# Kernel tuning notes

Measured on AMD Instinct MI355X. Metric: run time of the kernel, lower is better.

## Reference

```python
import jax, jax.numpy as jnp
import numpy as np

MAX_RES = 10.0  # max_residue_magnitude
DG = 16         # deformable_groups
KH = KW = 3
PAD = 1


def conv3x3(x, w, b):
    y = jax.lax.conv_general_dilated(x, w, window_strides=(1, 1), padding='SAME',
                                     dimension_numbers=('NCHW', 'OIHW', 'NCHW'))
    return y + b[None, :, None, None]


def lrelu(x):
    return jnp.where(x >= 0, x, 0.1 * x)


def deform_conv2d(x, offset, mask, weight, bias):
    # x: [B,C,H,W]; offset: [B,2*DG*K,H,W] as (dy,dx) pairs; mask: [B,DG*K,H,W]
    B, C, H, W = x.shape
    Cout, Cin, kh, kw = weight.shape
    K = kh * kw
    Cg = C // DG
    ky, kx = jnp.meshgrid(jnp.arange(kh), jnp.arange(kw), indexing='ij')
    ky = (ky.reshape(K) - PAD).astype(x.dtype)
    kx = (kx.reshape(K) - PAD).astype(x.dtype)
    off = offset.reshape(B, DG, K, 2, H, W)
    m = mask.reshape(B, DG, K, H, W)
    hh = jnp.arange(H, dtype=x.dtype)[None, None, None, :, None]
    ww = jnp.arange(W, dtype=x.dtype)[None, None, None, None, :]
    ys = hh + ky[None, None, :, None, None] + off[:, :, :, 0]  # [B,DG,K,H,W]
    xs = ww + kx[None, None, :, None, None] + off[:, :, :, 1]
    xg = x.reshape(B, DG, Cg, H, W)

    def sample_one(img, ys1, xs1):
        # img [Cg,H,W], ys1/xs1 [K,H,W]; bilinear with zero outside
        y0 = jnp.floor(ys1)
        x0 = jnp.floor(xs1)
        wy = ys1 - y0
        wx = xs1 - x0
        y0i = y0.astype(jnp.int32)
        x0i = x0.astype(jnp.int32)

        def g(yi, xi):
            valid = ((yi >= 0) & (yi < H) & (xi >= 0) & (xi < W)).astype(img.dtype)
            yc = jnp.clip(yi, 0, H - 1)
            xc = jnp.clip(xi, 0, W - 1)
            return img[:, yc, xc] * valid[None]  # [Cg,K,H,W]

        v00 = g(y0i, x0i)
        v01 = g(y0i, x0i + 1)
        v10 = g(y0i + 1, x0i)
        v11 = g(y0i + 1, x0i + 1)
        return (v00 * (1 - wy) * (1 - wx) + v01 * (1 - wy) * wx
                + v10 * wy * (1 - wx) + v11 * wy * wx)

    sampled = jax.vmap(jax.vmap(sample_one))(xg, ys, xs)     # [B,DG,Cg,K,H,W]
    sampled = sampled * m[:, :, None]
    sampled = sampled.reshape(B, C, K, H, W)
    wk = weight.reshape(Cout, Cin, K)
    out = jnp.einsum('bckhw,ock->bohw', sampled, wk)
    return out + bias[None, :, None, None]


def setup_inputs() -> dict:
    key = jax.random.key(0)
    ks = jax.random.split(key, 12)
    B, C, H, W = 4, 64, 128, 128
    s = lambda fan: 1.0 / np.sqrt(fan)
    inp = {
        'x': jax.random.normal(ks[0], (B, C, H, W), jnp.float32),
        'x_flow_warped': jax.random.normal(ks[1], (B, C, H, W), jnp.float32),
        'x_current': jax.random.normal(ks[2], (B, C, H, W), jnp.float32),
        'flow': jax.random.normal(ks[3], (B, 2, H, W), jnp.float32) * 2.0,
        'w_off1': jax.random.normal(ks[4], (64, 130, 3, 3), jnp.float32) * s(130 * 9),
        'b_off1': jnp.zeros((64,), jnp.float32),
        'w_off2': jax.random.normal(ks[5], (64, 64, 3, 3), jnp.float32) * s(64 * 9),
        'b_off2': jnp.zeros((64,), jnp.float32),
        'w_off3': jax.random.normal(ks[6], (64, 64, 3, 3), jnp.float32) * s(64 * 9),
        'b_off3': jnp.zeros((64,), jnp.float32),
        'w_off4': jax.random.normal(ks[7], (432, 64, 3, 3), jnp.float32) * s(64 * 9),
        'b_off4': jnp.zeros((432,), jnp.float32),
        'dcn_w': jax.random.normal(ks[8], (64, 64, 3, 3), jnp.float32) * s(64 * 9),
        'dcn_b': jnp.zeros((64,), jnp.float32),
    }
    return inp


def reference(x, x_flow_warped, x_current, flow,
              w_off1, b_off1, w_off2, b_off2, w_off3, b_off3, w_off4, b_off4,
              dcn_w, dcn_b):
    # conv_offset stack on cat(x_flow_warpeds + [x_current] + flows)
    feat = jnp.concatenate([x_flow_warped, x_current, flow], axis=1)  # [B,130,H,W]
    h = lrelu(conv3x3(feat, w_off1, b_off1))
    h = lrelu(conv3x3(h, w_off2, b_off2))
    h = lrelu(conv3x3(h, w_off3, b_off3))
    out = conv3x3(h, w_off4, b_off4)  # [B,432,H,W]
    o1, o2, mask = jnp.split(out, 3, axis=1)  # each [B,144,H,W]
    offset = MAX_RES * jnp.tanh(jnp.concatenate([o1, o2], axis=1))  # [B,288,H,W]
    flow_yx = flow[:, ::-1]  # flip(1): (dx,dy) -> (dy,dx)
    offset = offset + jnp.tile(flow_yx, (1, offset.shape[1] // 2, 1, 1))
    mask = jax.nn.sigmoid(mask)
    return deform_conv2d(x, offset, mask, dcn_w, dcn_b)
```

## Files before the change

### kernel.cpp

```cpp
#include <hip/hip_runtime.h>
#include <hip/hip_fp16.h>
#include <math.h>

#define HH 128
#define WW 128
#define BB 4
#define HWSZ (HH*WW)
#define PW 130
#define PSZ (PW*PW)

typedef _Float16 half_t;
typedef half_t half2v __attribute__((ext_vector_type(2)));
typedef half_t half4v __attribute__((ext_vector_type(4)));
typedef half_t half8 __attribute__((ext_vector_type(8)));
typedef float  f32x16 __attribute__((ext_vector_type(16)));

__device__ __forceinline__ float lrelu_f(float v) { return v >= 0.0f ? v : 0.1f * v; }
__device__ __forceinline__ float tanh_fast(float x) {
    float t = __expf(2.0f * x);
    return (t - 1.0f) / (t + 1.0f);
}
__device__ __forceinline__ float sigmoid_fast(float x) {
    return 1.0f / (1.0f + __expf(-x));
}

__global__ __launch_bounds__(256)
void pack_a0_k(const float* __restrict__ xfw, const float* __restrict__ xc,
               const float* __restrict__ flow, half_t* __restrict__ a0)
{
    __shared__ float s[64][145];
    const int tid = threadIdx.x;
    const int p0 = blockIdx.x * 64;
    for (int i = tid; i < 64 * 144; i += 256) {
        int c = i >> 6, px = i & 63;
        int pp = p0 + px;
        float v = 0.0f;
        if (pp < BB * PSZ) {
            int b = pp / PSZ; int p = pp - b * PSZ;
            int yy = p / PW, xx = p - yy * PW;
            if (yy >= 1 && yy <= HH && xx >= 1 && xx <= WW) {
                int pi = (yy - 1) * WW + (xx - 1);
                if (c < 64)       v = xfw[(size_t)(b*64 + c) * HWSZ + pi];
                else if (c < 128) v = xc [(size_t)(b*64 + c - 64) * HWSZ + pi];
                else if (c < 130) v = flow[(size_t)(b*2 + c - 128) * HWSZ + pi];
            }
        }
        s[px][c] = v;
    }
    __syncthreads();
    for (int i = tid; i < 64 * 144; i += 256) {
        int px = i / 144, c = i - px * 144;
        int pp = p0 + px;
        if (pp < BB * PSZ)
            a0[(size_t)pp * 144 + c] = (half_t)s[px][c];
    }
}

__global__ __launch_bounds__(256)
void zero_border_k(half_t* __restrict__ hbuf)
{
    int idx = blockIdx.x * 256 + threadIdx.x;
    if (idx >= 2064 * 8) return;
    int chunk = idx & 7; int bp = idx >> 3;
    int b = bp / 516;     int rr = bp - b * 516;
    int yy, xx;
    if (rr < 130)      { yy = 0;        xx = rr; }
    else if (rr < 260) { yy = 129;      xx = rr - 130; }
    else if (rr < 388) { yy = rr - 259; xx = 0; }
    else               { yy = rr - 387; xx = 129; }
    size_t base = ((size_t)(b * PSZ + yy * PW + xx)) * 64 + chunk * 8;
    half8 z = {(half_t)0.f,(half_t)0.f,(half_t)0.f,(half_t)0.f,
               (half_t)0.f,(half_t)0.f,(half_t)0.f,(half_t)0.f};
    *(half8*)(hbuf + base) = z;
}

__global__ __launch_bounds__(256)
void pack_w_k(const float* __restrict__ w, half_t* __restrict__ wp,
              int OC, int CIN, int OCP, int CINP, int NKC, int OCB)
{
    int idx = blockIdx.x * 256 + threadIdx.x;
    if (idx >= OCP * CINP * 9) return;
    int j   = idx & 7;
    int r   = idx >> 3;
    int ocw = r % OCB;  r /= OCB;
    int ks  = r & 1;    r >>= 1;
    int tap = r % 9;    r /= 9;
    int kc  = r % NKC;
    int ocg = r / NKC;
    int oc  = ocg * OCB + ocw;
    int cin = kc * 16 + ks * 8 + j;
    float v = (oc < OC && cin < CIN) ? w[((size_t)oc * CIN + cin) * 9 + tap] : 0.0f;
    wp[idx] = (half_t)v;
}

__global__ __launch_bounds__(256)
void pack_dw_k(const float* __restrict__ dw, half_t* __restrict__ Bp)
{
    int idx = blockIdx.x * 256 + threadIdx.x;
    if (idx >= 16 * 3 * 64 * 16) return;
    int kj = idx & 15;
    int oc = (idx >> 4) & 63;
    int r  = idx >> 10;
    int ks = r % 3;
    int dg = r / 3;
    int tap = ks * 4 + (kj >> 2);
    int cg  = kj & 3;
    float v = (tap < 9) ? dw[((size_t)oc * 64 + dg*4 + cg) * 9 + tap] : 0.0f;
    Bp[idx] = (half_t)v;
}

__global__ __launch_bounds__(256)
void pack_xt_k(const float* __restrict__ x, half_t* __restrict__ xTh)
{
    __shared__ float s[64][65];
    const int tid = threadIdx.x;
    const int p0 = blockIdx.x * 64;
    const int b = p0 >> 14, pp = p0 & 16383;
    for (int i = tid; i < 4096; i += 256) {
        int c = i >> 6, p = i & 63;
        s[p][c] = x[((size_t)(b*64 + c) << 14) + pp + p];
    }
    __syncthreads();
    for (int i = tid; i < 1024; i += 256) {
        int dg = i >> 6, p = i & 63;
        half4v v = { (half_t)s[p][dg*4+0], (half_t)s[p][dg*4+1],
                     (half_t)s[p][dg*4+2], (half_t)s[p][dg*4+3] };
        *(half4v*)(xTh + ((size_t)(dg*BB + b) * HWSZ + pp + p) * 4) = v;
    }
}

template<int CINP, int MT, int EPI, int NT>
__global__ __launch_bounds__(256, (EPI == 1 ? 8 : 4))
void conv_mfma_k(const half_t* __restrict__ A, const half_t* __restrict__ Wp,
                 const float* __restrict__ bias, void* __restrict__ outv,
                 int OC, const float* __restrict__ flow)
{
    constexpr int NKC   = CINP / 16;
    constexpr int PSTR  = 24;
    constexpr int PROWS = 8 * MT;
    constexpr int HALO  = (PROWS + 2) * 18;
    constexpr int NCH_A = HALO * 2;
    constexpr int OCB   = NT * 32;
    constexpr int NCH_B = 9 * 2 * OCB;
    const int tid  = threadIdx.x;
    const int lane = tid & 63;
    const int wv   = tid >> 6;
    const int b     = blockIdx.y;
    const int patch = blockIdx.x;
    const int y0 = (patch >> 3) * PROWS;
    const int x0 = (patch & 7) * 16;
    const int ocBase = blockIdx.z * OCB;

    __shared__ __align__(16) half_t s_a[HALO * PSTR];
    __shared__ __align__(16) half_t s_b[NCH_B * 8];

    f32x16 acc[MT][NT];
#pragma unroll
    for (int mt = 0; mt < MT; ++mt)
#pragma unroll
        for (int nt = 0; nt < NT; ++nt)
#pragma unroll
            for (int r = 0; r < 16; ++r) acc[mt][nt][r] = 0.0f;

    const int m     = lane & 31;
    const int klane = lane >> 5;
    const int row0  = wv * 2 * MT + (m >> 4);
    const int pxx   = m & 15;
    int abase[MT];
#pragma unroll
    for (int mt = 0; mt < MT; ++mt)
        abase[mt] = ((row0 + 2*mt) * 18 + pxx) * PSTR + klane * 8;

    const half_t* Ab = A + (size_t)b * PSZ * CINP;

    for (int kc = 0; kc < NKC; ++kc) {
        __syncthreads();
        {
            const half_t* wsrc = Wp + ((size_t)(blockIdx.z * NKC + kc) * NCH_B) * 8;
#pragma unroll
            for (int i = tid; i < NCH_B; i += 256)
                __builtin_amdgcn_global_load_lds(
                    (const __attribute__((address_space(1))) void*)(wsrc + i * 8),
                    (__attribute__((address_space(3))) void*)(s_b + i * 8),
                    16, 0, 0);
        }
        for (int i = tid; i < NCH_A; i += 256) {
            int pix = i >> 1, half = i & 1;
            int hy = pix / 18, hx = pix - hy * 18;
            const half_t* src = Ab + (size_t)((y0 + hy) * PW + x0 + hx) * CINP
                                + kc * 16 + half * 8;
            *(half8*)(s_a + pix * PSTR + half * 8) = *(const half8*)src;
        }
        __syncthreads();

#pragma unroll
        for (int tap = 0; tap < 9; ++tap) {
            const int aoff = ((tap / 3) * 18 + (tap % 3)) * PSTR;
            half8 Bh[NT];
#pragma unroll
            for (int nt = 0; nt < NT; ++nt)
                Bh[nt] = *(const half8*)(s_b + (((tap*2 + klane)*OCB + nt*32 + m)*8));
#pragma unroll
            for (int mt = 0; mt < MT; ++mt) {
                half8 Ah = *(const half8*)(s_a + abase[mt] + aoff);
#pragma unroll
                for (int nt = 0; nt < NT; ++nt)
                    acc[mt][nt] = __builtin_amdgcn_mfma_f32_32x32x16_f16(Ah, Bh[nt], acc[mt][nt], 0,0,0);
            }
        }
    }

    if (EPI == 0) {
#pragma unroll
        for (int nt = 0; nt < NT; ++nt) {
            const int oc = ocBase + nt * 32 + m;
            const float bv = bias[oc];
#pragma unroll
            for (int mt = 0; mt < MT; ++mt) {
#pragma unroll
                for (int r = 0; r < 16; ++r) {
                    const int row = (r & 3) + 8 * (r >> 2) + 4 * klane;
                    const int pyy = wv * 2 * MT + mt * 2 + (row >> 4);
                    const int gy = y0 + pyy, gx = x0 + (row & 15);
                    float v = lrelu_f(acc[mt][nt][r] + bv);
                    half_t* o = (half_t*)outv;
                    o[((size_t)(b * PSZ + (gy + 1) * PW + (gx + 1))) * 64 + oc] = (half_t)v;
                }
            }
        }
    } else {
        constexpr int EPC = 32 * PROWS * 2;
        half_t* s_ep = s_b;
        half_t* o = (half_t*)outv;
#pragma unroll
        for (int nt = 0; nt < NT; ++nt) {
            __syncthreads();
            const int oc = ocBase + nt * 32 + m;
            const float bv = (oc < OC) ? bias[oc] : 0.0f;
#pragma unroll
            for (int mt = 0; mt < MT; ++mt) {
#pragma unroll
                for (int r = 0; r < 16; ++r) {
                    const int row = (r & 3) + 8 * (r >> 2) + 4 * klane;
                    const int pyy = wv * 2 * MT + mt * 2 + (row >> 4);
                    const int gxl = row & 15;
                    float v = acc[mt][nt][r] + bv;
                    if (oc < 288) {
                        const int fch = (oc & 1) ^ 1;
                        float fl = flow[(size_t)(b*2 + fch) * HWSZ + (y0+pyy) * WW + (x0+gxl)];
                        v = 10.0f * tanh_fast(v) + fl;
                    } else {
                        v = sigmoid_fast(v);
                    }
                    s_ep[m * 264 + pyy * 16 + gxl] = (half_t)v;
                }
            }
            __syncthreads();
            for (int c = tid; c < EPC; c += 256) {
                int ocl = c / (PROWS * 2), rem = c % (PROWS * 2);
                int row = rem >> 1, hf = rem & 1;
                int ocg = ocBase + nt * 32 + ocl;
                if (ocg < OC) {
                    half8 vv = *(const half8*)(s_ep + ocl * 264 + row * 16 + hf * 8);
                    *(half8*)(o + ((size_t)(b * 432 + ocg) << 14) + (y0 + row) * 128 + x0 + hf * 8) = vv;
                }
            }
        }
    }
}

__global__ __launch_bounds__(256, 4)
void dcn_mfma_k(const half_t* __restrict__ xTh, const __half* __restrict__ off4,
                const half_t* __restrict__ Bp, const float* __restrict__ bias,
                float* __restrict__ out, half_t* __restrict__ p1h)
{
    constexpr int HLO = 24;
    constexpr int WR  = 4 + 2 * HLO;
    constexpr int WC  = 32 + 2 * HLO;
    constexpr int NWIN = WR * WC;
    __shared__ __align__(16) char smem[40960];
    half4v* s_x = (half4v*)smem;
    float*  s_t = (float*)smem;
    half_t* s_o = (half_t*)(smem + 33792);

    const int tid   = threadIdx.x;
    const int lane  = tid & 63;
    const int wv    = tid >> 6;
    const int klane = lane >> 5;
    const int m     = lane & 31;
    const int zz    = blockIdx.x;
    const int b     = zz >> 1;
    const int dgbase = (zz & 1) * 8;
    const int tx0 = blockIdx.y * 32, ty0 = blockIdx.z * 4;
    const int py = ty0 + wv;
    const int px = tx0 + m;
    const int pixloc = wv * 32 + m;

    const __half* offb = off4 + (size_t)b * 432 * HWSZ;

    f32x16 acc[2];
#pragma unroll
    for (int nt = 0; nt < 2; ++nt)
#pragma unroll
        for (int r = 0; r < 16; ++r) acc[nt][r] = 0.0f;

    for (int dgi = 0; dgi < 8; ++dgi) {
        const int dg = dgbase + dgi;
        const half_t* xdg = xTh + ((size_t)(dg * BB + b) * HWSZ) * 4;
        __syncthreads();
        for (int i = tid; i < NWIN; i += 256) {
            int wr = i / WC, wc = i - wr * WC;
            int ry = ty0 - HLO + wr;
            int cx = tx0 - HLO + wc;
            half4v v = {};
            if ((unsigned)ry < (unsigned)HH && (unsigned)cx < (unsigned)WW)
                v = *(const half4v*)(xdg + ((size_t)ry * WW + cx) * 4);
            s_x[i] = v;
        }
        for (int i = tid; i < 27 * 16; i += 256) {
            int c = i >> 4, sub = i & 15;
            int row = sub >> 2, q = sub & 3;
            int gch = (c < 18) ? (18 * dg + c) : (288 + 9 * dg + (c - 18));
            const __half* src = offb + (size_t)gch * HWSZ + (ty0 + row) * WW + tx0 + q * 8;
            *(half8*)(s_o + c * 132 + row * 32 + q * 8) = *(const half8*)src;
        }
        __syncthreads();

        const half_t* bbase = Bp + (size_t)(dg * 3) * 64 * 16;
#pragma unroll
        for (int ks = 0; ks < 3; ++ks) {
            half2v svp[2][2] = {};
#pragma unroll
            for (int tt = 0; tt < 2; ++tt) {
                const int tap = ks * 4 + klane * 2 + tt;
                if (tap < 9) {
                    float oy = (float)s_o[(2*tap    ) * 132 + pixloc];
                    float ox = (float)s_o[(2*tap + 1) * 132 + pixloc];
                    float mk = (float)s_o[(18 + tap ) * 132 + pixloc];
                    float ys = (float)(py + tap / 3 - 1) + oy;
                    float xs = (float)(px + tap % 3 - 1) + ox;
                    float y0f = floorf(ys), x0f = floorf(xs);
                    float wy = ys - y0f,    wx = xs - x0f;
                    int y0 = (int)y0f, x0i = (int)x0f;
                    float a0 = (1.0f - wy) * mk, a1 = wy * mk;
                    float w00 = a0 * (1.0f - wx), w01 = a0 * wx;
                    float w10 = a1 * (1.0f - wx), w11 = a1 * wx;
                    const int wr0 = y0  - (ty0 - HLO);
                    const int wc0 = x0i - (tx0 - HLO);
                    half4v c00, c01, c10, c11;
                    if ((unsigned)wr0 < (unsigned)(WR - 1) &&
                        (unsigned)wc0 < (unsigned)(WC - 1)) {
                        const half4v* pw = s_x + wr0 * WC + wc0;
                        c00 = pw[0];  c01 = pw[1];
                        c10 = pw[WC]; c11 = pw[WC + 1];
                    } else {
                        int y1 = y0 + 1, x1 = x0i + 1;
                        float fy0 = (y0  >= 0 && y0  < HH) ? 1.0f : 0.0f;
                        float fy1 = (y1  >= 0 && y1  < HH) ? 1.0f : 0.0f;
                        float fx0 = (x0i >= 0 && x0i < WW) ? 1.0f : 0.0f;
                        float fx1 = (x1  >= 0 && x1  < WW) ? 1.0f : 0.0f;
                        int yc0 = min(max(y0, 0), HH-1), yc1 = min(max(y1, 0), HH-1);
                        int xc0 = min(max(x0i,0), WW-1), xc1 = min(max(x1, 0), WW-1);
                        w00 *= fy0 * fx0; w01 *= fy0 * fx1;
                        w10 *= fy1 * fx0; w11 *= fy1 * fx1;
                        c00 = *(const half4v*)(xdg + ((size_t)yc0 * WW + xc0) * 4);
                        c01 = *(const half4v*)(xdg + ((size_t)yc0 * WW + xc1) * 4);
                        c10 = *(const half4v*)(xdg + ((size_t)yc1 * WW + xc0) * 4);
                        c11 = *(const half4v*)(xdg + ((size_t)yc1 * WW + xc1) * 4);
                    }
                    half_t h00 = (half_t)w00, h01 = (half_t)w01;
                    half_t h10 = (half_t)w10, h11 = (half_t)w11;
                    half2v W00 = {h00, h00}, W01 = {h01, h01};
                    half2v W10 = {h10, h10}, W11 = {h11, h11};
                    half2v lo = __builtin_shufflevector(c00, c00, 0, 1) * W00
                              + __builtin_shufflevector(c01, c01, 0, 1) * W01
                              + __builtin_shufflevector(c10, c10, 0, 1) * W10
                              + __builtin_shufflevector(c11, c11, 0, 1) * W11;
                    half2v hi = __builtin_shufflevector(c00, c00, 2, 3) * W00
                              + __builtin_shufflevector(c01, c01, 2, 3) * W01
                              + __builtin_shufflevector(c10, c10, 2, 3) * W10
                              + __builtin_shufflevector(c11, c11, 2, 3) * W11;
                    svp[tt][0] = lo; svp[tt][1] = hi;
                }
            }
            half8 a;
            a[0] = svp[0][0][0]; a[1] = svp[0][0][1];
            a[2] = svp[0][1][0]; a[3] = svp[0][1][1];
            a[4] = svp[1][0][0]; a[5] = svp[1][0][1];
            a[6] = svp[1][1][0]; a[7] = svp[1][1][1];
#pragma unroll
            for (int nt = 0; nt < 2; ++nt) {
                half8 Bh = *(const half8*)(bbase + ((size_t)(ks*64 + nt*32 + m)) * 16 + klane*8);
                acc[nt] = __builtin_amdgcn_mfma_f32_32x32x16_f16(a, Bh, acc[nt], 0,0,0);
            }
        }
        __syncthreads();
    }

    if (dgbase == 0) {
#pragma unroll
        for (int nt = 0; nt < 2; ++nt) {
            const int oc = nt * 32 + m;
            const float bv = bias[oc];
#pragma unroll
            for (int r = 0; r < 16; ++r) {
                const int row = (r & 3) + 8 * (r >> 2) + 4 * klane;
                s_t[oc * 132 + wv * 32 + row] = acc[nt][r] + bv;
            }
        }
        __syncthreads();
        for (int c = tid; c < 2048; c += 256) {
            int ocl = c >> 5, rem = c & 31, row = rem >> 3, q = rem & 7;
            float4 v = *(const float4*)(s_t + ocl * 132 + row * 32 + q * 4);
            *(float4*)(out + ((size_t)(b*64 + ocl) << 14) + (ty0 + row) * 128 + tx0 + q * 4) = v;
        }
    } else {
#pragma unroll
        for (int nt = 0; nt < 2; ++nt) {
            const int oc = nt * 32 + m;
#pragma unroll
            for (int r = 0; r < 16; ++r) {
                const int row = (r & 3) + 8 * (r >> 2) + 4 * klane;
                s_t[oc * 132 + wv * 32 + row] = acc[nt][r];
            }
        }
        __syncthreads();
        for (int c = tid; c < 2048; c += 256) {
            int ocl = c >> 5, rem = c & 31, row = rem >> 3, q = rem & 7;
            float4 v = *(const float4*)(s_t + ocl * 132 + row * 32 + q * 4);
            half4v h = {(half_t)v.x, (half_t)v.y, (half_t)v.z, (half_t)v.w};
            *(half4v*)(p1h + ((size_t)(b*64 + ocl) << 14) + (ty0 + row) * 128 + tx0 + q * 4) = h;
        }
    }
}

__global__ __launch_bounds__(256)
void add_partial_k(float* __restrict__ out, const half_t* __restrict__ p1h)
{
    const int N4 = BB * 64 * HWSZ / 4;
    for (int i = blockIdx.x * 256 + threadIdx.x; i < N4; i += gridDim.x * 256) {
        float4 o = *(const float4*)(out + (size_t)i * 4);
        half4v p = *(const half4v*)(p1h + (size_t)i * 4);
        o.x += (float)p[0]; o.y += (float)p[1];
        o.z += (float)p[2]; o.w += (float)p[3];
        *(float4*)(out + (size_t)i * 4) = o;
    }
}

extern "C" void kernel_launch(void* const* d_in, const int* in_sizes, int n_in,
                              void* d_out, int out_size, void* d_ws, size_t ws_size,
                              hipStream_t stream)
{
    const float* x    = (const float*)d_in[0];
    const float* xfw  = (const float*)d_in[1];
    const float* xc   = (const float*)d_in[2];
    const float* flow = (const float*)d_in[3];
    const float* w1 = (const float*)d_in[4];  const float* b1 = (const float*)d_in[5];
    const float* w2 = (const float*)d_in[6];  const float* b2 = (const float*)d_in[7];
    const float* w3 = (const float*)d_in[8];  const float* b3 = (const float*)d_in[9];
    const float* w4 = (const float*)d_in[10]; const float* b4 = (const float*)d_in[11];
    const float* dw = (const float*)d_in[12]; const float* db = (const float*)d_in[13];

    char* wsb = (char*)d_ws;
    const size_t off4_bytes = (size_t)BB * 432 * HWSZ * 2;
    __half* off4 = (__half*)wsb;
    half_t* A0   = (half_t*)wsb;
    half_t* h2p  = (half_t*)wsb;
    char* p = wsb + off4_bytes;
    half_t* h1p = (half_t*)p;
    half_t* xTh = (half_t*)h1p;
    half_t* p1h = (half_t*)((char*)h1p + (size_t)BB * 64 * HWSZ * 2);
                               p += (size_t)BB * PSZ * 2 * 64 * 2;
    half_t* wp1 = (half_t*)p;  p += (size_t)64  * 144 * 9 * 2;
    half_t* wp2 = (half_t*)p;  p += (size_t)64  * 64  * 9 * 2;
    half_t* wp3 = (half_t*)p;  p += (size_t)64  * 64  * 9 * 2;
    half_t* wp4 = (half_t*)p;  p += (size_t)448 * 64  * 9 * 2;
    half_t* Bp  = (half_t*)p;  p += (size_t)16 * 3 * 64 * 16 * 2;

    zero_border_k<<<(2064*8 + 255)/256, 256, 0, stream>>>(h1p);
    pack_w_k<<<(64*144*9 + 255)/256, 256, 0, stream>>>(w1, wp1, 64, 130, 64, 144, 9, 64);
    pack_w_k<<<(64*64*9  + 255)/256, 256, 0, stream>>>(w2, wp2, 64, 64, 64, 64, 4, 64);
    pack_w_k<<<(64*64*9  + 255)/256, 256, 0, stream>>>(w3, wp3, 64, 64, 64, 64, 4, 64);
    pack_w_k<<<(448*64*9 + 255)/256, 256, 0, stream>>>(w4, wp4, 432, 64, 448, 64, 4, 64);
    pack_dw_k<<<(16*3*64*16 + 255)/256, 256, 0, stream>>>(dw, Bp);
    pack_a0_k<<<(BB*PSZ + 63)/64, 256, 0, stream>>>(xfw, xc, flow, A0);

    conv_mfma_k<144,1,0,2><<<dim3(128, BB, 1), 256, 0, stream>>>(A0,  wp1, b1, h1p, 64,  nullptr);
    zero_border_k<<<(2064*8 + 255)/256, 256, 0, stream>>>(h2p);
    conv_mfma_k<64, 1,0,2><<<dim3(128, BB, 1), 256, 0, stream>>>(h1p, wp2, b2, h2p, 64,  nullptr);
    conv_mfma_k<64, 1,0,2><<<dim3(128, BB, 1), 256, 0, stream>>>(h2p, wp3, b3, h1p, 64,  nullptr);
    conv_mfma_k<64, 1,1,2><<<dim3(128, BB, 7), 256, 0, stream>>>(h1p, wp4, b4, off4, 432, flow);
    pack_xt_k<<<BB * HWSZ / 64, 256, 0, stream>>>(x, xTh);

    dcn_mfma_k<<<dim3(BB*2, 4, 32), 256, 0, stream>>>(xTh, off4, Bp, db, (float*)d_out, p1h);
    add_partial_k<<<2048, 256, 0, stream>>>((float*)d_out, p1h);
}
```

Baseline: 328.0 us.

## Register-prefetch next deformable group's window and offsets during MFMA compute

```diff
diff --git a/kernel.cpp b/kernel.cpp
--- a/kernel.cpp
+++ b/kernel.cpp
@@ -304,27 +304,63 @@
 #pragma unroll
         for (int r = 0; r < 16; ++r) acc[nt][r] = 0.0f;
 
+    half4v rx[17];
+    half8  ro[2];
+
+    auto issue_stage = [&](int dg) {
+        const half_t* xdg = xTh + ((size_t)(dg * BB + b) * HWSZ) * 4;
+#pragma unroll
+        for (int it = 0; it < 17; ++it) {
+            int i = it * 256 + tid;
+            half4v v = {};
+            if (i < NWIN) {
+                int wr = i / WC, wc = i - wr * WC;
+                int ry = ty0 - HLO + wr;
+                int cx = tx0 - HLO + wc;
+                if ((unsigned)ry < (unsigned)HH && (unsigned)cx < (unsigned)WW)
+                    v = *(const half4v*)(xdg + ((size_t)ry * WW + cx) * 4);
+            }
+            rx[it] = v;
+        }
+#pragma unroll
+        for (int it = 0; it < 2; ++it) {
+            int i = it * 256 + tid;
+            half8 v = {};
+            if (i < 27 * 16) {
+                int c = i >> 4, sub = i & 15;
+                int row = sub >> 2, q = sub & 3;
+                int gch = (c < 18) ? (18 * dg + c) : (288 + 9 * dg + (c - 18));
+                v = *(const half8*)((const half_t*)offb + (size_t)gch * HWSZ
+                                    + (ty0 + row) * WW + tx0 + q * 8);
+            }
+            ro[it] = v;
+        }
+    };
+    auto write_stage = [&]() {
+#pragma unroll
+        for (int it = 0; it < 17; ++it) {
+            int i = it * 256 + tid;
+            if (i < NWIN) s_x[i] = rx[it];
+        }
+#pragma unroll
+        for (int it = 0; it < 2; ++it) {
+            int i = it * 256 + tid;
+            if (i < 27 * 16) {
+                int c = i >> 4, sub = i & 15;
+                int row = sub >> 2, q = sub & 3;
+                *(half8*)(s_o + c * 132 + row * 32 + q * 8) = ro[it];
+            }
+        }
+    };
+
+    issue_stage(dgbase);
     for (int dgi = 0; dgi < 8; ++dgi) {
         const int dg = dgbase + dgi;
         const half_t* xdg = xTh + ((size_t)(dg * BB + b) * HWSZ) * 4;
         __syncthreads();
-        for (int i = tid; i < NWIN; i += 256) {
-            int wr = i / WC, wc = i - wr * WC;
-            int ry = ty0 - HLO + wr;
-            int cx = tx0 - HLO + wc;
-            half4v v = {};
-            if ((unsigned)ry < (unsigned)HH && (unsigned)cx < (unsigned)WW)
-                v = *(const half4v*)(xdg + ((size_t)ry * WW + cx) * 4);
-            s_x[i] = v;
-        }
-        for (int i = tid; i < 27 * 16; i += 256) {
-            int c = i >> 4, sub = i & 15;
-            int row = sub >> 2, q = sub & 3;
-            int gch = (c < 18) ? (18 * dg + c) : (288 + 9 * dg + (c - 18));
-            const __half* src = offb + (size_t)gch * HWSZ + (ty0 + row) * WW + tx0 + q * 8;
-            *(half8*)(s_o + c * 132 + row * 32 + q * 8) = *(const half8*)src;
-        }
+        write_stage();
         __syncthreads();
+        if (dgi < 7) issue_stage(dg + 1);
 
         const half_t* bbase = Bp + (size_t)(dg * 3) * 64 * 16;
 #pragma unroll
@@ -394,8 +430,8 @@
                 acc[nt] = __builtin_amdgcn_mfma_f32_32x32x16_f16(a, Bh, acc[nt], 0,0,0);
             }
         }
-        __syncthreads();
-    }
+    }
+    __syncthreads();
 
     if (dgbase == 0) {
 #pragma unroll
```

Result: slower. 360.8 us (+10.0%).
